# Kernel optimization log

Measured on AMD Instinct MI355X. Metric: run time of the kernel, lower is better.

Reference implementation:

```python
import jax, jax.numpy as jnp
import numpy as np

NUM_BLOCKS = 16  # 4x4 grid of 2x2 blocks over the 8x8 matrix
E_BLK, H_BLK = 4, 2
E_CROSS, H_CROSS = 64, 8
VOCAB = 32000
LN_EPS = 1e-5


def _mha(x, Wqkv, bqkv, Wo, bo, nheads):
    """torch nn.MultiheadAttention (batch_first, self-attn, eval mode).
    Returns (out [B,T,E], attn weights averaged over heads [B,T,T])."""
    B, T, E = x.shape
    Dh = E // nheads
    qkv = x @ Wqkv.T + bqkv                      # [B,T,3E]
    q, k, v = jnp.split(qkv, 3, axis=-1)
    sp = lambda t: t.reshape(B, T, nheads, Dh).transpose(0, 2, 1, 3)  # [B,H,T,Dh]
    q, k, v = sp(q), sp(k), sp(v)
    scale = 1.0 / float(np.sqrt(Dh))
    scores = jnp.einsum('bhqd,bhkd->bhqk', q, k) * scale
    attn = jax.nn.softmax(scores, axis=-1)
    out = jnp.einsum('bhqk,bhkd->bhqd', attn, v).transpose(0, 2, 1, 3).reshape(B, T, E)
    return out @ Wo.T + bo, attn.mean(axis=1)


def _layernorm(x, g, b):
    mu = x.mean(-1, keepdims=True)
    var = x.var(-1, keepdims=True)
    return (x - mu) * jax.lax.rsqrt(var + LN_EPS) * g + b


def _to_blocks(M):
    # [B,T,8,8] -> [B,T,16,4]; block i = (row_blk*4+col_blk), 2x2 flattened row-major
    B, T = M.shape[:2]
    return jnp.transpose(M.reshape(B, T, 4, 2, 4, 2), (0, 1, 2, 4, 3, 5)).reshape(B, T, 16, 4)


def _from_blocks(x):
    # [B,T,16,4] -> [B,T,8,8]
    B, T = x.shape[:2]
    return jnp.transpose(x.reshape(B, T, 4, 4, 2, 2), (0, 1, 2, 4, 3, 5)).reshape(B, T, 8, 8)


def setup_inputs() -> dict:
    key = jax.random.key(0)
    ks = jax.random.split(key, 24)
    B, T = 4, 1024
    s = 0.05
    return {
        'M': jax.random.normal(ks[0], (B, T, 8, 8), jnp.float32),
        'token_ids': jax.random.randint(ks[1], (B, T), 0, VOCAB, jnp.int64),
        # 16 per-block MHA param sets (stacked)
        'Wqkv_blk': jax.random.normal(ks[2], (NUM_BLOCKS, 3 * E_BLK, E_BLK), jnp.float32) * s,
        'bqkv_blk': jnp.zeros((NUM_BLOCKS, 3 * E_BLK), jnp.float32),
        'Wo_blk': jax.random.normal(ks[3], (NUM_BLOCKS, E_BLK, E_BLK), jnp.float32) * s,
        'bo_blk': jnp.zeros((NUM_BLOCKS, E_BLK), jnp.float32),
        # cross-block MHA
        'Wqkv_c': jax.random.normal(ks[4], (3 * E_CROSS, E_CROSS), jnp.float32) * s,
        'bqkv_c': jnp.zeros((3 * E_CROSS,), jnp.float32),
        'Wo_c': jax.random.normal(ks[5], (E_CROSS, E_CROSS), jnp.float32) * s,
        'bo_c': jnp.zeros((E_CROSS,), jnp.float32),
        # FFN 64 -> 256 -> 64
        'W1': jax.random.normal(ks[6], (256, 64), jnp.float32) * s,
        'b1': jnp.zeros((256,), jnp.float32),
        'W2': jax.random.normal(ks[7], (64, 256), jnp.float32) * s,
        'b2': jnp.zeros((64,), jnp.float32),
        # LayerNorms
        'g1': jnp.ones((64,), jnp.float32), 'be1': jnp.zeros((64,), jnp.float32),
        'g2': jnp.ones((64,), jnp.float32), 'be2': jnp.zeros((64,), jnp.float32),
        # DynamicBlockSensitivity params
        'sens_emb': jax.random.normal(ks[8], (VOCAB, NUM_BLOCKS), jnp.float32) * s,
        'sens_alpha': jax.random.normal(ks[9], (NUM_BLOCKS,), jnp.float32) * s,
    }


def reference(M, token_ids, Wqkv_blk, bqkv_blk, Wo_blk, bo_blk,
              Wqkv_c, bqkv_c, Wo_c, bo_c, W1, b1, W2, b2,
              g1, be1, g2, be2, sens_emb, sens_alpha):
    B, T = M.shape[:2]
    blocks = _to_blocks(M)                                # [B,T,16,4]
    x_blk = jnp.moveaxis(blocks, 2, 0)                    # [16,B,T,4]
    blk_out, _ = jax.vmap(lambda x, W, b, Wo, bo: _mha(x, W, b, Wo, bo, H_BLK))(
        x_blk, Wqkv_blk, bqkv_blk, Wo_blk, bo_blk)        # [16,B,T,4]
    all_blocks = jnp.moveaxis(blk_out, 0, 2).reshape(B, T, 64)
    cross_out, attn_w = _mha(all_blocks, Wqkv_c, bqkv_c, Wo_c, bo_c, H_CROSS)
    all_blocks = _layernorm(all_blocks + cross_out, g1, be1)
    ffn = jax.nn.gelu(all_blocks @ W1.T + b1, approximate=False) @ W2.T + b2
    all_blocks = _layernorm(all_blocks + ffn, g2, be2)
    # Dynamic block sensitivity: token embedding + attention-received modulation
    attn_recv = attn_w.mean(axis=1)                       # [B,T] attention each token receives
    sens = jax.nn.sigmoid(sens_emb[token_ids] + attn_recv[..., None] * sens_alpha)  # [B,T,16]
    new_blocks = blocks + (all_blocks.reshape(B, T, 16, 4) - blocks) * sens[..., None]
    return _from_blocks(new_blocks)
```

## Files before the change

### kernel.cpp

```cpp
#include <hip/hip_runtime.h>
#include <hip/hip_bf16.h>
#include <math.h>

#define BB 4
#define TT 1024
#define BT 4096

#define OFF_BLOCKS 0
#define OFF_QKVB   262144
#define OFF_RECVP  262144
#define OFF_ALLB   1048576
#define OFF_QKVC   1310720
#define OFF_LC     2097152
#define OFF_ACCC   2129920
#define OFF_LN1    2396160
#define OFF_PARAMS 2658304
#define WS_FLOATS  2708624

#define P_W1T    0
#define P_W2T    16384
#define P_WQCT   32768
#define P_WOCT   45056
#define P_WOBLK  49152
#define P_BOBLK  49408
#define P_BQC    49472
#define P_BOC    49664
#define P_G1     49728
#define P_BE1    49792
#define P_B1     49856
#define P_B2     50112
#define P_G2     50176
#define P_BE2    50240
#define P_SAL    50304
#define P_TOTAL  50320

__device__ inline float rcpf(float x) { return __builtin_amdgcn_rcpf(x); }

typedef _Float16 h2 __attribute__((ext_vector_type(2)));
typedef __fp16   fh2 __attribute__((ext_vector_type(2)));
typedef _Float16 h8v __attribute__((ext_vector_type(8)));
typedef float    f4v __attribute__((ext_vector_type(4)));

__device__ inline uint pkh(float a, float b) {
#if __has_builtin(__builtin_amdgcn_cvt_pkrtz)
  fh2 r = __builtin_amdgcn_cvt_pkrtz(a, b);
  return __builtin_bit_cast(uint, r);
#else
  h2 r = { (_Float16)a, (_Float16)b };
  return __builtin_bit_cast(uint, r);
#endif
}
__device__ inline h2 toh2(uint u) { return __builtin_bit_cast(h2, u); }

__device__ inline float dot2h(h2 a, h2 b, float c) {
#if __has_builtin(__builtin_amdgcn_fdot2)
  return __builtin_amdgcn_fdot2(a, b, c, false);
#else
  return c + (float)a.x * (float)b.x + (float)a.y * (float)b.y;
#endif
}

__device__ inline bool detect_bf16(const void* M) {
  const unsigned short* h = (const unsigned short*)M;
  unsigned short v = h[threadIdx.x & 63];
  int e = (v >> 7) & 0xff;
  unsigned long long m = __ballot((e >= 90) && (e <= 141));
  return __popcll(m) >= 58;
}

template <bool ISBF>
__device__ inline float ldf(const void* p, int i) {
  if (ISBF) return __bfloat162float(((const __hip_bfloat16*)p)[i]);
  else      return ((const float*)p)[i];
}

template <bool ISBF>
__device__ void prep2_body(
    const void* M, const void* Wqkv_blk, const void* bqkv_blk,
    const void* W1, const void* W2, const void* Wqkv_c, const void* Wo_c,
    const void* Wo_blk, const void* bo_blk, const void* bqkv_c, const void* bo_c,
    const void* g1, const void* be1, const void* b1, const void* b2,
    const void* g2, const void* be2, const void* sens_al,
    float* blocks, float* qkv_blk, float* params) {
  if (blockIdx.x < 256) {
    int g = blockIdx.x * 256 + threadIdx.x;
    int i = g >> 12, bt = g & 4095;
    int rb = i >> 2, cb = i & 3;
    float x[4];
    #pragma unroll
    for (int r = 0; r < 2; ++r)
      #pragma unroll
      for (int c = 0; c < 2; ++c)
        x[r*2+c] = ldf<ISBF>(M, bt*64 + (rb*2+r)*8 + cb*2 + c);
    float* bo = blocks + bt*64 + i*4;
    #pragma unroll
    for (int j = 0; j < 4; ++j) bo[j] = x[j];
    float* o = qkv_blk + (i*BT + bt) * 12;
    #pragma unroll
    for (int c = 0; c < 12; ++c) {
      float a = ldf<ISBF>(bqkv_blk, i*12 + c);
      #pragma unroll
      for (int j = 0; j < 4; ++j) a += ldf<ISBF>(Wqkv_blk, i*48 + c*4 + j) * x[j];
      o[c] = a;
    }
  } else {
    for (int o = (blockIdx.x - 256)*256 + threadIdx.x; o < P_TOTAL; o += 16*256) {
      float v;
      if      (o < 16384) { int j = o >> 8, h2_ = o & 255; v = ldf<ISBF>(W1, h2_*64 + j); }
      else if (o < 32768) { int q = o - 16384; int k = q >> 6, j = q & 63; v = ldf<ISBF>(W2, j*256 + k); }
      else if (o < 45056) { int q = o - 32768; int j = q / 192, c = q % 192; v = ldf<ISBF>(Wqkv_c, c*64 + j); }
      else if (o < 49152) { int q = o - 45056; int m = q >> 6, j = q & 63; v = ldf<ISBF>(Wo_c, j*64 + m); }
      else if (o < 49408) v = ldf<ISBF>(Wo_blk, o - 49152);
      else if (o < 49472) v = ldf<ISBF>(bo_blk, o - 49408);
      else if (o < 49664) v = ldf<ISBF>(bqkv_c, o - 49472);
      else if (o < 49728) v = ldf<ISBF>(bo_c,   o - 49664);
      else if (o < 49792) v = ldf<ISBF>(g1,     o - 49728);
      else if (o < 49856) v = ldf<ISBF>(be1,    o - 49792);
      else if (o < 50112) v = ldf<ISBF>(b1,     o - 49856);
      else if (o < 50176) v = ldf<ISBF>(b2,     o - 50112);
      else if (o < 50240) v = ldf<ISBF>(g2,     o - 50176);
      else if (o < 50304) v = ldf<ISBF>(be2,    o - 50240);
      else                v = ldf<ISBF>(sens_al, o - 50304);
      params[o] = v;
    }
  }
}

__global__ void __launch_bounds__(256) k_prep3(
    const void* __restrict__ M, const void* __restrict__ Wqkv_blk,
    const void* __restrict__ bqkv_blk,
    const void* __restrict__ W1, const void* __restrict__ W2,
    const void* __restrict__ Wqkv_c, const void* __restrict__ Wo_c,
    const void* __restrict__ Wo_blk, const void* __restrict__ bo_blk,
    const void* __restrict__ bqkv_c, const void* __restrict__ bo_c,
    const void* __restrict__ g1, const void* __restrict__ be1,
    const void* __restrict__ b1, const void* __restrict__ b2,
    const void* __restrict__ g2, const void* __restrict__ be2,
    const void* __restrict__ sens_al,
    float* __restrict__ blocks, float* __restrict__ qkv_blk,
    float* __restrict__ params) {
  if (detect_bf16(M))
    prep2_body<true >(M, Wqkv_blk, bqkv_blk, W1, W2, Wqkv_c, Wo_c, Wo_blk, bo_blk,
                      bqkv_c, bo_c, g1, be1, b1, b2, g2, be2, sens_al,
                      blocks, qkv_blk, params);
  else
    prep2_body<false>(M, Wqkv_blk, bqkv_blk, W1, W2, Wqkv_c, Wo_c, Wo_blk, bo_blk,
                      bqkv_c, bo_c, g1, be1, b1, b2, g2, be2, sens_al,
                      blocks, qkv_blk, params);
}

__global__ void __launch_bounds__(256) k_blk4(
    const float* __restrict__ qkv_blk,
    const float* __restrict__ params,
    float* __restrict__ all_blocks) {
  __shared__ __align__(16) uint lds[9236];
  uint* kvu = lds;
  uint* vt  = lds + 4096;
  ushort* vt16 = (ushort*)vt;
  int bid = blockIdx.x;
  int qc = bid & 15, b = (bid >> 4) & 3, i = bid >> 6;
  int tid = threadIdx.x;
  int wv = tid >> 6, lane = tid & 63;
  int lq = lane & 15, g = lane >> 4;
  const float* slab = qkv_blk + (size_t)(i*BT + b*TT) * 12;
  #pragma unroll
  for (int rr = 0; rr < 4; ++rr) {
    int r = tid + rr*256;
    const float4* rp = (const float4*)(slab + (size_t)r*12);
    float4 x1 = rp[1], x2 = rp[2];
    uint v01 = pkh(x2.x, x2.y), v23 = pkh(x2.z, x2.w);
    *(uint4*)(kvu + r*4) = make_uint4(pkh(x1.x,x1.y), pkh(x1.z,x1.w), v01, v23);
    vt16[0*1032 + r] = (ushort)(v01 & 0xffffu);
    vt16[1*1032 + r] = (ushort)(v01 >> 16);
    vt16[2*1032 + r] = (ushort)(v23 & 0xffffu);
    vt16[3*1032 + r] = (ushort)(v23 >> 16);
    vt16[4*1032 + r] = (ushort)0x3C00;
  }
  int qrow = qc*64 + wv*16 + lq;
  float4 qv = *(const float4*)(slab + (size_t)qrow*12);
  const float S2L = 0.70710678f * 1.44269504f;
  uint pq01 = pkh(qv.x*S2L, qv.y*S2L);
  uint pq23 = pkh(qv.z*S2L, qv.w*S2L);
  uint4 bq0u = make_uint4(g == 0 ? pq01 : 0u, 0u, 0u, 0u);
  uint4 bq1u = make_uint4(0u, g == 0 ? pq23 : 0u, 0u, 0u);
  h8v B0 = __builtin_bit_cast(h8v, bq0u);
  h8v B1 = __builtin_bit_cast(h8v, bq1u);
  __syncthreads();
  uint* pt0 = lds + 6676 + (wv*2 + 0)*320;
  uint* pt1 = lds + 6676 + (wv*2 + 1)*320;
  f4v acc0 = {0.f, 0.f, 0.f, 0.f};
  f4v acc1 = {0.f, 0.f, 0.f, 0.f};
  for (int c = 0; c < 32; ++c) {
    int kb = c*32;
    #pragma unroll
    for (int t = 0; t < 2; ++t) {
      uint4 aku = *(const uint4*)(kvu + (size_t)(kb + t*16 + lq)*4);
      h8v AK = __builtin_bit_cast(h8v, aku);
      f4v z = {0.f, 0.f, 0.f, 0.f};
      f4v s0 = __builtin_amdgcn_mfma_f32_16x16x32_f16(AK, B0, z, 0, 0, 0);
      f4v s1 = __builtin_amdgcn_mfma_f32_16x16x32_f16(AK, B1, z, 0, 0, 0);
      uint a01 = pkh(exp2f(s0[0]), exp2f(s0[1]));
      uint a23 = pkh(exp2f(s0[2]), exp2f(s0[3]));
      uint c01 = pkh(exp2f(s1[0]), exp2f(s1[1]));
      uint c23 = pkh(exp2f(s1[2]), exp2f(s1[3]));
      *(uint2*)(pt0 + lq*20 + t*8 + g*2) = make_uint2(a01, a23);
      *(uint2*)(pt1 + lq*20 + t*8 + g*2) = make_uint2(c01, c23);
    }
    uint4 avu = make_uint4(0u, 0u, 0u, 0u);
    if (lq < 5) avu = *(const uint4*)(vt + (size_t)lq*516 + c*16 + g*4);
    h8v AV = __builtin_bit_cast(h8v, avu);
    h8v BP0 = __builtin_bit_cast(h8v, *(const uint4*)(pt0 + lq*20 + g*4));
    h8v BP1 = __builtin_bit_cast(h8v, *(const uint4*)(pt1 + lq*20 + g*4));
    acc0 = __builtin_amdgcn_mfma_f32_16x16x32_f16(AV, BP0, acc0, 0, 0, 0);
    acc1 = __builtin_amdgcn_mfma_f32_16x16x32_f16(AV, BP1, acc1, 0, 0, 0);
  }
  float l0 = __shfl(acc0[0], 16 + lq);
  float l1 = __shfl(acc1[0], 16 + lq);
  if (g == 0) {
    float inv0 = rcpf(l0), inv1 = rcpf(l1);
    float o[4] = { acc0[0]*inv0, acc0[1]*inv0, acc1[2]*inv1, acc1[3]*inv1 };
    const float* pWo = params + P_WOBLK + i*16;
    float4 outv;
    #pragma unroll
    for (int j = 0; j < 4; ++j) {
      float a = params[P_BOBLK + i*4 + j];
      #pragma unroll
      for (int m2 = 0; m2 < 4; ++m2) a += pWo[j*4 + m2] * o[m2];
      ((float*)&outv)[j] = a;
    }
    *(float4*)(all_blocks + (size_t)(b*TT + qrow)*64 + i*4) = outv;
  }
}

__global__ void __launch_bounds__(256) k_qkv_c2(
    const float* __restrict__ all_blocks,
    const float* __restrict__ params,
    float* __restrict__ qkv_c) {
  __shared__ float w[12288];
  __shared__ float xs[256];
  int tid = threadIdx.x;
  int t0 = blockIdx.x * 4;
  {
    const float4* src = (const float4*)(params + P_WQCT);
    float4* dst = (float4*)w;
    #pragma unroll
    for (int i = tid; i < 3072; i += 256) dst[i] = src[i];
  }
  xs[tid] = all_blocks[t0*64 + tid];
  __syncthreads();
  int tt = tid >> 6, lane = tid & 63;
  int t = t0 + tt;
  const float* x = xs + tt*64;
  float a0 = params[P_BQC + lane];
  float a1 = params[P_BQC + 64 + lane];
  float a2 = params[P_BQC + 128 + lane];
  #pragma unroll 8
  for (int j = 0; j < 64; ++j) {
    const float* r = w + j*192;
    float xj = x[j];
    a0 += r[lane]       * xj;
    a1 += r[64 + lane]  * xj;
    a2 += r[128 + lane] * xj;
  }
  float* o = qkv_c + (size_t)t*192;
  o[lane] = a0; o[64 + lane] = a1; o[128 + lane] = a2;
}

__global__ void __launch_bounds__(1024) k_cross10(
    const float* __restrict__ qkv_c,
    float* __restrict__ acc_c,
    float* __restrict__ recv_part) {
  __shared__ __align__(16) uint lds[23680];
  uint*  Ku   = lds;
  uint*  Vu   = lds + 4096;
  float* red  = (float*)(lds + 4096);
  float* rcmb = (float*)(lds + 4096);
  uint*  qb_  = lds + 22656;
  int bid = blockIdx.x;
  int qt = bid & 7, h = (bid >> 3) & 7, b = bid >> 6;
  int tid = threadIdx.x;
  int wv = __builtin_amdgcn_readfirstlane(tid) >> 6;
  int ql = tid & 63;
  int h8 = h*8;
  const float* base = qkv_c + (size_t)b*TT*192;
  {
    int r = tid;
    const float4* kp = (const float4*)(base + (size_t)r*192 + 64 + h8);
    const float4* vp = (const float4*)(base + (size_t)r*192 + 128 + h8);
    float4 k0 = kp[0], k1 = kp[1], v0 = vp[0], v1 = vp[1];
    *(uint4*)(Ku + r*4) = make_uint4(pkh(k0.x,k0.y), pkh(k0.z,k0.w),
                                     pkh(k1.x,k1.y), pkh(k1.z,k1.w));
    *(uint4*)(Vu + r*4) = make_uint4(pkh(v0.x,v0.y), pkh(v0.z,v0.w),
                                     pkh(v1.x,v1.y), pkh(v1.z,v1.w));
  }
  int qa = qt*128 + ql, qbq = qa + 64;
  const float SCL = 0.35355339f * 1.44269504f;
  uint qa01,qa23,qa45,qa67, qb01,qb23,qb45,qb67;
  {
    const float4* pa = (const float4*)(base + (size_t)qa*192 + h8);
    const float4* pb = (const float4*)(base + (size_t)qbq*192 + h8);
    float4 a0 = pa[0], a1 = pa[1], b0 = pb[0], b1 = pb[1];
    qa01 = pkh(a0.x*SCL, a0.y*SCL); qa23 = pkh(a0.z*SCL, a0.w*SCL);
    qa45 = pkh(a1.x*SCL, a1.y*SCL); qa67 = pkh(a1.z*SCL, a1.w*SCL);
    qb01 = pkh(b0.x*SCL, b0.y*SCL); qb23 = pkh(b0.z*SCL, b0.w*SCL);
    qb45 = pkh(b1.x*SCL, b1.y*SCL); qb67 = pkh(b1.z*SCL, b1.w*SCL);
  }
  __syncthreads();
  float la = 0.f, lb = 0.f, aca[8], acb[8];
  #pragma unroll
  for (int c = 0; c < 8; ++c) { aca[c] = 0.f; acb[c] = 0.f; }
  int kbeg = wv*64;
  #pragma unroll 4
  for (int k = kbeg; k < kbeg + 64; ++k) {
    uint4 kk = *(const uint4*)(Ku + k*4);
    uint4 vv = *(const uint4*)(Vu + k*4);
    h2 k01 = toh2(kk.x), k23 = toh2(kk.y), k45 = toh2(kk.z), k67 = toh2(kk.w);
    float sa = dot2h(toh2(qa01),k01, dot2h(toh2(qa23),k23, 0.f))
             + dot2h(toh2(qa45),k45, dot2h(toh2(qa67),k67, 0.f));
    float sb = dot2h(toh2(qb01),k01, dot2h(toh2(qb23),k23, 0.f))
             + dot2h(toh2(qb45),k45, dot2h(toh2(qb67),k67, 0.f));
    float pa = exp2f(sa);
    float pb = exp2f(sb);
    la += pa; lb += pb;
    h2 v01 = toh2(vv.x), v23 = toh2(vv.y), v45 = toh2(vv.z), v67 = toh2(vv.w);
    aca[0] += pa*(float)v01.x; aca[1] += pa*(float)v01.y;
    aca[2] += pa*(float)v23.x; aca[3] += pa*(float)v23.y;
    aca[4] += pa*(float)v45.x; aca[5] += pa*(float)v45.y;
    aca[6] += pa*(float)v67.x; aca[7] += pa*(float)v67.y;
    acb[0] += pb*(float)v01.x; acb[1] += pb*(float)v01.y;
    acb[2] += pb*(float)v23.x; acb[3] += pb*(float)v23.y;
    acb[4] += pb*(float)v45.x; acb[5] += pb*(float)v45.y;
    acb[6] += pb*(float)v67.x; acb[7] += pb*(float)v67.y;
  }
  __syncthreads();
  {
    float* ra = red + ql*145 + wv*9;
    ra[0] = la;
    #pragma unroll
    for (int c = 0; c < 8; ++c) ra[1+c] = aca[c];
    float* rb = red + (ql+64)*145 + wv*9;
    rb[0] = lb;
    #pragma unroll
    for (int c = 0; c < 8; ++c) rb[1+c] = acb[c];
    if (wv == 0) {
      *(uint4*)(qb_ + ql*8)      = make_uint4(qa01, qa23, qa45, qa67);
      *(uint4*)(qb_ + (ql+64)*8) = make_uint4(qb01, qb23, qb45, qb67);
    }
  }
  __syncthreads();
  if (tid < 128) {
    float ls = 0.f, as[8];
    #pragma unroll
    for (int c = 0; c < 8; ++c) as[c] = 0.f;
    #pragma unroll
    for (int w = 0; w < 16; ++w) {
      const float* p = red + tid*145 + w*9;
      ls += p[0];
      #pragma unroll
      for (int c = 0; c < 8; ++c) as[c] += p[1+c];
    }
    float invl = rcpf(ls);
    int q2 = qt*128 + tid;
    int idx = (b*8 + h)*TT + q2;
    float4 o0 = { as[0]*invl, as[1]*invl, as[2]*invl, as[3]*invl };
    float4 o1 = { as[4]*invl, as[5]*invl, as[6]*invl, as[7]*invl };
    float4* op = (float4*)(acc_c + (size_t)idx*8);
    op[0] = o0; op[1] = o1;
    ((float*)(qb_ + tid*8))[4] = -__log2f(ls);
  }
  __syncthreads();
  {
    int qq = wv >> 2, g = wv & 3;
    int p = g*64 + ql;
    uint4 ka = *(const uint4*)(Ku + p*4);
    uint4 kb = *(const uint4*)(Ku + (p+256)*4);
    uint4 kc = *(const uint4*)(Ku + (p+512)*4);
    uint4 kd = *(const uint4*)(Ku + (p+768)*4);
    float r0 = 0.f, r1 = 0.f, r2 = 0.f, r3 = 0.f;
    const uint* qrow = qb_ + qq*32*8;
    #pragma unroll 4
    for (int q = 0; q < 32; ++q) {
      uint4 q4 = *(const uint4*)(qrow + q*8);
      float mq = __uint_as_float(qrow[q*8 + 4]);
      h2 Q0 = toh2(q4.x), Q1 = toh2(q4.y), Q2 = toh2(q4.z), Q3 = toh2(q4.w);
      float s0 = dot2h(Q0,toh2(ka.x), dot2h(Q1,toh2(ka.y), 0.f))
               + dot2h(Q2,toh2(ka.z), dot2h(Q3,toh2(ka.w), 0.f));
      float s1 = dot2h(Q0,toh2(kb.x), dot2h(Q1,toh2(kb.y), 0.f))
               + dot2h(Q2,toh2(kb.z), dot2h(Q3,toh2(kb.w), 0.f));
      float s2 = dot2h(Q0,toh2(kc.x), dot2h(Q1,toh2(kc.y), 0.f))
               + dot2h(Q2,toh2(kc.z), dot2h(Q3,toh2(kc.w), 0.f));
      float s3 = dot2h(Q0,toh2(kd.x), dot2h(Q1,toh2(kd.y), 0.f))
               + dot2h(Q2,toh2(kd.z), dot2h(Q3,toh2(kd.w), 0.f));
      r0 += exp2f(s0 + mq);
      r1 += exp2f(s1 + mq);
      r2 += exp2f(s2 + mq);
      r3 += exp2f(s3 + mq);
    }
    rcmb[(p      )*4 + qq] = r0;
    rcmb[(p + 256)*4 + qq] = r1;
    rcmb[(p + 512)*4 + qq] = r2;
    rcmb[(p + 768)*4 + qq] = r3;
  }
  __syncthreads();
  {
    int k = tid;
    float4 v = *(const float4*)(rcmb + k*4);
    int src = h*8 + qt;
    recv_part[((size_t)(b*1024 + k))*64 + src] = v.x + v.y + v.z + v.w;
  }
}

__global__ void __launch_bounds__(256) k_fin(
    const float* __restrict__ all_blocks,
    const float* __restrict__ acc_c,
    const float* __restrict__ params,
    float* __restrict__ ln1) {
  __shared__ float pvs[4*64];
  int tt = threadIdx.x >> 6, j = threadIdx.x & 63;
  int t = blockIdx.x*4 + tt;
  int b = t >> 10, tl = t & 1023;
  int h = j >> 3;
  int idx = (b*8 + h)*TT + tl;
  pvs[tt*64 + j] = acc_c[idx*8 + (j & 7)];
  __syncthreads();
  float a = params[P_BOC + j];
  const float* WoT = params + P_WOCT;
  const float* p = pvs + tt*64;
  #pragma unroll 8
  for (int m = 0; m < 64; ++m) a += WoT[m*64 + j] * p[m];
  float x = all_blocks[t*64 + j] + a;
  float s = x, s2 = x*x;
  #pragma unroll
  for (int off = 32; off; off >>= 1) { s += __shfl_xor(s, off); s2 += __shfl_xor(s2, off); }
  float mu  = s  * (1.f/64.f);
  float var = s2 * (1.f/64.f) - mu*mu;
  float y = (x - mu) * rsqrtf(var + 1e-5f) * params[P_G1 + j] + params[P_BE1 + j];
  ln1[t*64 + j] = y;
}

template <bool ISBF>
__device__ void ffn_body(
    const float* ln1, const float* params, const float* blocks,
    const int* tok32, const float* recv_part, const void* sens_emb, void* out,
    float* w, float* ld2, float* hbuf) {
  int tid = threadIdx.x;
  int t0 = blockIdx.x * 8;
  int wv = tid >> 6, lane = tid & 63;
  float recv;
  {
    int t = t0 + wv, b = t >> 10, k = t & 1023;
    const float* rp = recv_part + ((size_t)(b*1024 + k))*64;
    float s = rp[lane];
    #pragma unroll
    for (int off = 32; off; off >>= 1) s += __shfl_xor(s, off);
    recv = s * (1.f/8192.f);
  }
  ld2[lane*8 + wv] = ln1[(t0 + wv)*64 + lane];
  {
    const float4* src = (const float4*)(params + P_W1T);
    float4* dst = (float4*)w;
    #pragma unroll
    for (int i = tid; i < 4096; i += 512) dst[i] = src[i];
  }
  __syncthreads();
  {
    int g = tid >> 8, u = tid & 255;
    float a0, a1, a2, a3;
    a0 = a1 = a2 = a3 = params[P_B1 + u];
    #pragma unroll 8
    for (int j = 0; j < 64; ++j) {
      float wj = w[j*256 + u];
      float4 xj = *(const float4*)(ld2 + j*8 + g*4);
      a0 += wj*xj.x; a1 += wj*xj.y; a2 += wj*xj.z; a3 += wj*xj.w;
    }
    float av[4] = {a0, a1, a2, a3};
    float4 hv;
    #pragma unroll
    for (int t2 = 0; t2 < 4; ++t2) {
      float v = av[t2];
      float u2 = 1.5957691f*v + 0.07135481f*v*v*v;
      ((float*)&hv)[t2] = v * rcpf(1.f + __expf(-u2));
    }
    *(float4*)(hbuf + u*8 + g*4) = hv;
  }
  __syncthreads();
  {
    const float4* src = (const float4*)(params + P_W2T);
    float4* dst = (float4*)w;
    #pragma unroll
    for (int i = tid; i < 4096; i += 512) dst[i] = src[i];
  }
  __syncthreads();
  float yp[8] = {0.f,0.f,0.f,0.f,0.f,0.f,0.f,0.f};
  {
    int j = lane, k0 = wv*32;
    #pragma unroll 8
    for (int k = k0; k < k0 + 32; ++k) {
      float wkj = w[k*64 + j];
      float4 h03 = *(const float4*)(hbuf + k*8);
      float4 h47 = *(const float4*)(hbuf + k*8 + 4);
      yp[0] += wkj*h03.x; yp[1] += wkj*h03.y; yp[2] += wkj*h03.z; yp[3] += wkj*h03.w;
      yp[4] += wkj*h47.x; yp[5] += wkj*h47.y; yp[6] += wkj*h47.z; yp[7] += wkj*h47.w;
    }
  }
  __syncthreads();
  float* red2 = w;
  {
    #pragma unroll
    for (int t2 = 0; t2 < 8; ++t2) red2[wv*520 + t2*64 + lane] = yp[t2];
  }
  __syncthreads();
  int j = lane;
  int tok = wv;
  int t = t0 + tok, b = t >> 10;
  float y = params[P_B2 + j];
  #pragma unroll
  for (int wq = 0; wq < 8; ++wq) y += red2[wq*520 + tok*64 + j];
  float z = ld2[j*8 + tok] + y;
  float s = z, s2 = z*z;
  #pragma unroll
  for (int off = 32; off; off >>= 1) { s += __shfl_xor(s, off); s2 += __shfl_xor(s2, off); }
  float mu  = s  * (1.f/64.f);
  float var = s2 * (1.f/64.f) - mu*mu;
  float y2 = (z - mu) * rsqrtf(var + 1e-5f) * params[P_G2 + j] + params[P_BE2 + j];
  bool is64 = ((tok32[1] | tok32[3] | tok32[5] | tok32[7]) == 0);
  int tk = is64 ? tok32[t*2] : tok32[t];
  int i = j >> 2, e = j & 3;
  float sv = ldf<ISBF>(sens_emb, tk*16 + i) + recv * params[P_SAL + i];
  float sg = rcpf(1.f + __expf(-sv));
  float blk = blocks[t*64 + j];
  float nb = blk + (y2 - blk) * sg;
  int rb = i >> 2, cb = i & 3, r = e >> 1, c = e & 1;
  int oidx = t*64 + (rb*2 + r)*8 + cb*2 + c;
  if (ISBF) ((__hip_bfloat16*)out)[oidx] = __float2bfloat16(nb);
  else      ((float*)out)[oidx] = nb;
}

__global__ void __launch_bounds__(512) k_ffn_out3(
    const void* __restrict__ M,
    const float* __restrict__ ln1,
    const float* __restrict__ params,
    const float* __restrict__ blocks,
    const int* __restrict__ tok32,
    const float* __restrict__ recv_part,
    const void* __restrict__ sens_emb,
    void* __restrict__ out) {
  __shared__ float w[16384];
  __shared__ float ld2[512];
  __shared__ float hbuf[2048];
  if (detect_bf16(M))
    ffn_body<true >(ln1, params, blocks, tok32, recv_part, sens_emb, out, w, ld2, hbuf);
  else
    ffn_body<false>(ln1, params, blocks, tok32, recv_part, sens_emb, out, w, ld2, hbuf);
}

extern "C" void kernel_launch(void* const* d_in, const int* in_sizes, int n_in,
                              void* d_out, int out_size, void* d_ws, size_t ws_size,
                              hipStream_t stream) {
  const void* M        = d_in[0];
  const int*  tok      = (const int*)d_in[1];
  const void* Wqkv_blk = d_in[2];
  const void* bqkv_blk = d_in[3];
  const void* Wo_blk   = d_in[4];
  const void* bo_blk   = d_in[5];
  const void* Wqkv_c   = d_in[6];
  const void* bqkv_c   = d_in[7];
  const void* Wo_c     = d_in[8];
  const void* bo_c     = d_in[9];
  const void* W1       = d_in[10];
  const void* b1       = d_in[11];
  const void* W2       = d_in[12];
  const void* b2       = d_in[13];
  const void* g1       = d_in[14];
  const void* be1      = d_in[15];
  const void* g2i      = d_in[16];
  const void* be2      = d_in[17];
  const void* sens_emb = d_in[18];
  const void* sens_al  = d_in[19];

  float* ws = (float*)d_ws;
  float* blocks    = ws + OFF_BLOCKS;
  float* qkv_blk   = ws + OFF_QKVB;
  float* recv_part = ws + OFF_RECVP;
  float* all_blk   = ws + OFF_ALLB;
  float* qkv_c     = ws + OFF_QKVC;
  float* acc_c     = ws + OFF_ACCC;
  float* ln1       = ws + OFF_LN1;
  float* params    = ws + OFF_PARAMS;

  k_prep3<<<272, 256, 0, stream>>>(M, Wqkv_blk, bqkv_blk, W1, W2, Wqkv_c, Wo_c,
                                   Wo_blk, bo_blk, bqkv_c, bo_c, g1, be1, b1, b2,
                                   g2i, be2, sens_al, blocks, qkv_blk, params);
  k_blk4<<<1024, 256, 0, stream>>>(qkv_blk, params, all_blk);
  k_qkv_c2<<<1024, 256, 0, stream>>>(all_blk, params, qkv_c);
  k_cross10<<<256, 1024, 0, stream>>>(qkv_c, acc_c, recv_part);
  k_fin<<<1024, 256, 0, stream>>>(all_blk, acc_c, params, ln1);
  k_ffn_out3<<<512, 512, 0, stream>>>(M, ln1, params, blocks, tok, recv_part,
                                      sens_emb, (void*)d_out);
}
```

Before: 208.0 us.

## Rewrite cross-block attention with MFMA f16 matrix instructions for QK and PV

Replaces the scalar fdot2-based cross attention kernel with one using 16x16x32 f16 MFMA for QK^T scores, PV accumulation (with a ones row in transposed V to get the softmax denominator), and the attention-received recomputation pass. The grid changes to 512 blocks of 256 threads, each handling 64 queries per (batch, head), and the per-source receive partials widen from 64 to 128 columns, with the consumer kernel updated to match. The aim is to move the dominant dot-product work onto matrix cores. The trade-off is wasted MFMA lanes from zero padding, since head dim 8 only fills a quarter of K, plus LDS round-trips for P and shuffle reductions.

```diff
diff --git a/kernel.cpp b/kernel.cpp
--- a/kernel.cpp
+++ b/kernel.cpp
@@ -51,14 +51,6 @@
 #endif
 }
 __device__ inline h2 toh2(uint u) { return __builtin_bit_cast(h2, u); }
-
-__device__ inline float dot2h(h2 a, h2 b, float c) {
-#if __has_builtin(__builtin_amdgcn_fdot2)
-  return __builtin_amdgcn_fdot2(a, b, c, false);
-#else
-  return c + (float)a.x * (float)b.x + (float)a.y * (float)b.y;
-#endif
-}
 
 __device__ inline bool detect_bf16(const void* M) {
   const unsigned short* h = (const unsigned short*)M;
@@ -266,147 +258,125 @@
   o[lane] = a0; o[64 + lane] = a1; o[128 + lane] = a2;
 }
 
-__global__ void __launch_bounds__(1024) k_cross10(
+__global__ void __launch_bounds__(256) k_cross11(
     const float* __restrict__ qkv_c,
     float* __restrict__ acc_c,
     float* __restrict__ recv_part) {
-  __shared__ __align__(16) uint lds[23680];
-  uint*  Ku   = lds;
-  uint*  Vu   = lds + 4096;
-  float* red  = (float*)(lds + 4096);
-  float* rcmb = (float*)(lds + 4096);
-  uint*  qb_  = lds + 22656;
+  __shared__ __align__(16) uint lds[14116];
+  uint* Ku = lds;
+  uint* Vt = lds + 4096;
+  ushort* vt16 = (ushort*)Vt;
+  float* rcv = (float*)(lds + 10020);
   int bid = blockIdx.x;
-  int qt = bid & 7, h = (bid >> 3) & 7, b = bid >> 6;
+  int h = bid & 7, b = (bid >> 3) & 3, qc = bid >> 5;
   int tid = threadIdx.x;
-  int wv = __builtin_amdgcn_readfirstlane(tid) >> 6;
-  int ql = tid & 63;
+  int wv = tid >> 6, lane = tid & 63;
+  int lq = lane & 15, g = lane >> 4;
   int h8 = h*8;
   const float* base = qkv_c + (size_t)b*TT*192;
-  {
-    int r = tid;
+  #pragma unroll
+  for (int rr = 0; rr < 4; ++rr) {
+    int r = tid + rr*256;
     const float4* kp = (const float4*)(base + (size_t)r*192 + 64 + h8);
     const float4* vp = (const float4*)(base + (size_t)r*192 + 128 + h8);
     float4 k0 = kp[0], k1 = kp[1], v0 = vp[0], v1 = vp[1];
     *(uint4*)(Ku + r*4) = make_uint4(pkh(k0.x,k0.y), pkh(k0.z,k0.w),
                                      pkh(k1.x,k1.y), pkh(k1.z,k1.w));
-    *(uint4*)(Vu + r*4) = make_uint4(pkh(v0.x,v0.y), pkh(v0.z,v0.w),
-                                     pkh(v1.x,v1.y), pkh(v1.z,v1.w));
-  }
-  int qa = qt*128 + ql, qbq = qa + 64;
+    uint v01 = pkh(v0.x,v0.y), v23 = pkh(v0.z,v0.w);
+    uint v45 = pkh(v1.x,v1.y), v67 = pkh(v1.z,v1.w);
+    vt16[0*1032 + r] = (ushort)(v01 & 0xffffu);
+    vt16[1*1032 + r] = (ushort)(v01 >> 16);
+    vt16[2*1032 + r] = (ushort)(v23 & 0xffffu);
+    vt16[3*1032 + r] = (ushort)(v23 >> 16);
+    vt16[4*1032 + r] = (ushort)(v45 & 0xffffu);
+    vt16[5*1032 + r] = (ushort)(v45 >> 16);
+    vt16[6*1032 + r] = (ushort)(v67 & 0xffffu);
+    vt16[7*1032 + r] = (ushort)(v67 >> 16);
+    vt16[8*1032 + r] = (ushort)0x3C00;
+  }
+  int q2 = qc*64 + wv*16 + lq;
   const float SCL = 0.35355339f * 1.44269504f;
-  uint qa01,qa23,qa45,qa67, qb01,qb23,qb45,qb67;
-  {
-    const float4* pa = (const float4*)(base + (size_t)qa*192 + h8);
-    const float4* pb = (const float4*)(base + (size_t)qbq*192 + h8);
-    float4 a0 = pa[0], a1 = pa[1], b0 = pb[0], b1 = pb[1];
-    qa01 = pkh(a0.x*SCL, a0.y*SCL); qa23 = pkh(a0.z*SCL, a0.w*SCL);
-    qa45 = pkh(a1.x*SCL, a1.y*SCL); qa67 = pkh(a1.z*SCL, a1.w*SCL);
-    qb01 = pkh(b0.x*SCL, b0.y*SCL); qb23 = pkh(b0.z*SCL, b0.w*SCL);
-    qb45 = pkh(b1.x*SCL, b1.y*SCL); qb67 = pkh(b1.z*SCL, b1.w*SCL);
-  }
-  __syncthreads();
-  float la = 0.f, lb = 0.f, aca[8], acb[8];
-  #pragma unroll
-  for (int c = 0; c < 8; ++c) { aca[c] = 0.f; acb[c] = 0.f; }
-  int kbeg = wv*64;
-  #pragma unroll 4
-  for (int k = kbeg; k < kbeg + 64; ++k) {
-    uint4 kk = *(const uint4*)(Ku + k*4);
-    uint4 vv = *(const uint4*)(Vu + k*4);
-    h2 k01 = toh2(kk.x), k23 = toh2(kk.y), k45 = toh2(kk.z), k67 = toh2(kk.w);
-    float sa = dot2h(toh2(qa01),k01, dot2h(toh2(qa23),k23, 0.f))
-             + dot2h(toh2(qa45),k45, dot2h(toh2(qa67),k67, 0.f));
-    float sb = dot2h(toh2(qb01),k01, dot2h(toh2(qb23),k23, 0.f))
-             + dot2h(toh2(qb45),k45, dot2h(toh2(qb67),k67, 0.f));
-    float pa = exp2f(sa);
-    float pb = exp2f(sb);
-    la += pa; lb += pb;
-    h2 v01 = toh2(vv.x), v23 = toh2(vv.y), v45 = toh2(vv.z), v67 = toh2(vv.w);
-    aca[0] += pa*(float)v01.x; aca[1] += pa*(float)v01.y;
-    aca[2] += pa*(float)v23.x; aca[3] += pa*(float)v23.y;
-    aca[4] += pa*(float)v45.x; aca[5] += pa*(float)v45.y;
-    aca[6] += pa*(float)v67.x; aca[7] += pa*(float)v67.y;
-    acb[0] += pb*(float)v01.x; acb[1] += pb*(float)v01.y;
-    acb[2] += pb*(float)v23.x; acb[3] += pb*(float)v23.y;
-    acb[4] += pb*(float)v45.x; acb[5] += pb*(float)v45.y;
-    acb[6] += pb*(float)v67.x; acb[7] += pb*(float)v67.y;
-  }
-  __syncthreads();
-  {
-    float* ra = red + ql*145 + wv*9;
-    ra[0] = la;
-    #pragma unroll
-    for (int c = 0; c < 8; ++c) ra[1+c] = aca[c];
-    float* rb = red + (ql+64)*145 + wv*9;
-    rb[0] = lb;
-    #pragma unroll
-    for (int c = 0; c < 8; ++c) rb[1+c] = acb[c];
-    if (wv == 0) {
-      *(uint4*)(qb_ + ql*8)      = make_uint4(qa01, qa23, qa45, qa67);
-      *(uint4*)(qb_ + (ql+64)*8) = make_uint4(qb01, qb23, qb45, qb67);
-    }
-  }
-  __syncthreads();
-  if (tid < 128) {
-    float ls = 0.f, as[8];
-    #pragma unroll
-    for (int c = 0; c < 8; ++c) as[c] = 0.f;
-    #pragma unroll
-    for (int w = 0; w < 16; ++w) {
-      const float* p = red + tid*145 + w*9;
-      ls += p[0];
-      #pragma unroll
-      for (int c = 0; c < 8; ++c) as[c] += p[1+c];
-    }
-    float invl = rcpf(ls);
-    int q2 = qt*128 + tid;
+  uint4 bqu = make_uint4(0u, 0u, 0u, 0u);
+  {
+    const float4* qp = (const float4*)(base + (size_t)q2*192 + h8);
+    float4 q0 = qp[0], q1 = qp[1];
+    if (g == 0)
+      bqu = make_uint4(pkh(q0.x*SCL, q0.y*SCL), pkh(q0.z*SCL, q0.w*SCL),
+                       pkh(q1.x*SCL, q1.y*SCL), pkh(q1.z*SCL, q1.w*SCL));
+  }
+  h8v BQ = __builtin_bit_cast(h8v, bqu);
+  __syncthreads();
+  uint* pt = lds + 8740 + wv*320;
+  const uint4 zu4 = make_uint4(0u, 0u, 0u, 0u);
+  f4v acc = {0.f, 0.f, 0.f, 0.f};
+  for (int c = 0; c < 32; ++c) {
+    #pragma unroll
+    for (int t = 0; t < 2; ++t) {
+      uint4 aku = (g == 0) ? *(const uint4*)(Ku + (size_t)(c*32 + t*16 + lq)*4) : zu4;
+      h8v AK = __builtin_bit_cast(h8v, aku);
+      f4v z = {0.f, 0.f, 0.f, 0.f};
+      f4v s = __builtin_amdgcn_mfma_f32_16x16x32_f16(AK, BQ, z, 0, 0, 0);
+      uint e01 = pkh(exp2f(s[0]), exp2f(s[1]));
+      uint e23 = pkh(exp2f(s[2]), exp2f(s[3]));
+      *(uint2*)(pt + lq*20 + t*8 + g*2) = make_uint2(e01, e23);
+    }
+    uint4 avu = (lq < 9) ? *(const uint4*)(Vt + (size_t)lq*516 + c*16 + g*4) : zu4;
+    h8v AV = __builtin_bit_cast(h8v, avu);
+    h8v BP = __builtin_bit_cast(h8v, *(const uint4*)(pt + lq*20 + g*4));
+    acc = __builtin_amdgcn_mfma_f32_16x16x32_f16(AV, BP, acc, 0, 0, 0);
+  }
+  float l = __shfl(acc[0], 32 + lq);
+  float invl = rcpf(l);
+  float mq = -__log2f(l);
+  {
     int idx = (b*8 + h)*TT + q2;
-    float4 o0 = { as[0]*invl, as[1]*invl, as[2]*invl, as[3]*invl };
-    float4 o1 = { as[4]*invl, as[5]*invl, as[6]*invl, as[7]*invl };
-    float4* op = (float4*)(acc_c + (size_t)idx*8);
-    op[0] = o0; op[1] = o1;
-    ((float*)(qb_ + tid*8))[4] = -__log2f(ls);
-  }
-  __syncthreads();
-  {
-    int qq = wv >> 2, g = wv & 3;
-    int p = g*64 + ql;
-    uint4 ka = *(const uint4*)(Ku + p*4);
-    uint4 kb = *(const uint4*)(Ku + (p+256)*4);
-    uint4 kc = *(const uint4*)(Ku + (p+512)*4);
-    uint4 kd = *(const uint4*)(Ku + (p+768)*4);
-    float r0 = 0.f, r1 = 0.f, r2 = 0.f, r3 = 0.f;
-    const uint* qrow = qb_ + qq*32*8;
-    #pragma unroll 4
-    for (int q = 0; q < 32; ++q) {
-      uint4 q4 = *(const uint4*)(qrow + q*8);
-      float mq = __uint_as_float(qrow[q*8 + 4]);
-      h2 Q0 = toh2(q4.x), Q1 = toh2(q4.y), Q2 = toh2(q4.z), Q3 = toh2(q4.w);
-      float s0 = dot2h(Q0,toh2(ka.x), dot2h(Q1,toh2(ka.y), 0.f))
-               + dot2h(Q2,toh2(ka.z), dot2h(Q3,toh2(ka.w), 0.f));
-      float s1 = dot2h(Q0,toh2(kb.x), dot2h(Q1,toh2(kb.y), 0.f))
-               + dot2h(Q2,toh2(kb.z), dot2h(Q3,toh2(kb.w), 0.f));
-      float s2 = dot2h(Q0,toh2(kc.x), dot2h(Q1,toh2(kc.y), 0.f))
-               + dot2h(Q2,toh2(kc.z), dot2h(Q3,toh2(kc.w), 0.f));
-      float s3 = dot2h(Q0,toh2(kd.x), dot2h(Q1,toh2(kd.y), 0.f))
-               + dot2h(Q2,toh2(kd.z), dot2h(Q3,toh2(kd.w), 0.f));
-      r0 += exp2f(s0 + mq);
-      r1 += exp2f(s1 + mq);
-      r2 += exp2f(s2 + mq);
-      r3 += exp2f(s3 + mq);
-    }
-    rcmb[(p      )*4 + qq] = r0;
-    rcmb[(p + 256)*4 + qq] = r1;
-    rcmb[(p + 512)*4 + qq] = r2;
-    rcmb[(p + 768)*4 + qq] = r3;
-  }
-  __syncthreads();
-  {
-    int k = tid;
-    float4 v = *(const float4*)(rcmb + k*4);
-    int src = h*8 + qt;
-    recv_part[((size_t)(b*1024 + k))*64 + src] = v.x + v.y + v.z + v.w;
+    if (g == 0) {
+      float4 o = { acc[0]*invl, acc[1]*invl, acc[2]*invl, acc[3]*invl };
+      *(float4*)(acc_c + (size_t)idx*8) = o;
+    } else if (g == 1) {
+      float4 o = { acc[0]*invl, acc[1]*invl, acc[2]*invl, acc[3]*invl };
+      *(float4*)(acc_c + (size_t)idx*8 + 4) = o;
+    }
+  }
+  float* rcvw = rcv + wv*1024;
+  for (int x = lane; x < 1024; x += 64) rcvw[x] = 0.f;
+  for (int c2 = 0; c2 < 64; ++c2) {
+    uint4 aku = (g == 0) ? *(const uint4*)(Ku + (size_t)(c2*16 + lq)*4) : zu4;
+    h8v AK = __builtin_bit_cast(h8v, aku);
+    f4v z = {0.f, 0.f, 0.f, 0.f};
+    f4v s = __builtin_amdgcn_mfma_f32_16x16x32_f16(AK, BQ, z, 0, 0, 0);
+    float p0 = exp2f(s[0] + mq);
+    float p1 = exp2f(s[1] + mq);
+    float p2 = exp2f(s[2] + mq);
+    float p3 = exp2f(s[3] + mq);
+    #pragma unroll
+    for (int off = 1; off < 16; off <<= 1) {
+      p0 += __shfl_xor(p0, off);
+      p1 += __shfl_xor(p1, off);
+      p2 += __shfl_xor(p2, off);
+      p3 += __shfl_xor(p3, off);
+    }
+    if (lq == 0) {
+      int kb2 = c2*16 + g*4;
+      rcvw[kb2 + 0] += p0;
+      rcvw[kb2 + 1] += p1;
+      rcvw[kb2 + 2] += p2;
+      rcvw[kb2 + 3] += p3;
+    }
+  }
+  __syncthreads();
+  {
+    int k = tid*4;
+    float4 a0 = *(const float4*)(rcv + 0*1024 + k);
+    float4 a1 = *(const float4*)(rcv + 1*1024 + k);
+    float4 a2 = *(const float4*)(rcv + 2*1024 + k);
+    float4 a3 = *(const float4*)(rcv + 3*1024 + k);
+    int src = h*16 + qc;
+    size_t bk = ((size_t)(b*1024 + k))*128 + src;
+    recv_part[bk      ] = a0.x + a1.x + a2.x + a3.x;
+    recv_part[bk + 128] = a0.y + a1.y + a2.y + a3.y;
+    recv_part[bk + 256] = a0.z + a1.z + a2.z + a3.z;
+    recv_part[bk + 384] = a0.w + a1.w + a2.w + a3.w;
   }
 }
 
@@ -449,8 +419,8 @@
   float recv;
   {
     int t = t0 + wv, b = t >> 10, k = t & 1023;
-    const float* rp = recv_part + ((size_t)(b*1024 + k))*64;
-    float s = rp[lane];
+    const float* rp = recv_part + ((size_t)(b*1024 + k))*128;
+    float s = rp[lane] + rp[lane + 64];
     #pragma unroll
     for (int off = 32; off; off >>= 1) s += __shfl_xor(s, off);
     recv = s * (1.f/8192.f);
@@ -593,7 +563,7 @@
                                    g2i, be2, sens_al, blocks, qkv_blk, params);
   k_blk4<<<1024, 256, 0, stream>>>(qkv_blk, params, all_blk);
   k_qkv_c2<<<1024, 256, 0, stream>>>(all_blk, params, qkv_c);
-  k_cross10<<<256, 1024, 0, stream>>>(qkv_c, acc_c, recv_part);
+  k_cross11<<<512, 256, 0, stream>>>(qkv_c, acc_c, recv_part);
   k_fin<<<1024, 256, 0, stream>>>(all_blk, acc_c, params, ln1);
   k_ffn_out3<<<512, 512, 0, stream>>>(M, ln1, params, blocks, tok, recv_part,
                                       sens_emb, (void*)d_out);
```

Measured after the change: 221.8 us. +6.6%, slower.

## Compute cross-attention QKV projection with fp16 MFMA over 16-token tiles

Applied to the files above, without the earlier changes.

Replaces the scalar fp32 QKV projection with a kernel that packs the weights to fp16 in LDS and uses 16x16x32 MFMA instructions, handling 16 tokens per block instead of 4. This cuts the per-block reload of the full weight matrix and the scalar FMA cost. In exchange, inputs and weights are rounded to fp16, which reduces accuracy, and each block still transposes and packs the weights itself.

```diff
diff --git a/kernel.cpp b/kernel.cpp
--- a/kernel.cpp
+++ b/kernel.cpp
@@ -232,38 +232,48 @@
   }
 }
 
-__global__ void __launch_bounds__(256) k_qkv_c2(
+__global__ void __launch_bounds__(256) k_qkv_c3(
     const float* __restrict__ all_blocks,
     const float* __restrict__ params,
     float* __restrict__ qkv_c) {
-  __shared__ float w[12288];
-  __shared__ float xs[256];
+  __shared__ __align__(16) uint wt[6912];
   int tid = threadIdx.x;
-  int t0 = blockIdx.x * 4;
-  {
-    const float4* src = (const float4*)(params + P_WQCT);
-    float4* dst = (float4*)w;
-    #pragma unroll
-    for (int i = tid; i < 3072; i += 256) dst[i] = src[i];
-  }
-  xs[tid] = all_blocks[t0*64 + tid];
-  __syncthreads();
-  int tt = tid >> 6, lane = tid & 63;
-  int t = t0 + tt;
-  const float* x = xs + tt*64;
-  float a0 = params[P_BQC + lane];
-  float a1 = params[P_BQC + 64 + lane];
-  float a2 = params[P_BQC + 128 + lane];
-  #pragma unroll 8
-  for (int j = 0; j < 64; ++j) {
-    const float* r = w + j*192;
-    float xj = x[j];
-    a0 += r[lane]       * xj;
-    a1 += r[64 + lane]  * xj;
-    a2 += r[128 + lane] * xj;
-  }
-  float* o = qkv_c + (size_t)t*192;
-  o[lane] = a0; o[64 + lane] = a1; o[128 + lane] = a2;
+  int wv = tid >> 6, lane = tid & 63;
+  int lq = lane & 15, g = lane >> 4;
+  for (int o = tid; o < 6144; o += 256) {
+    int c = o % 192, jp = o / 192;
+    float w0 = params[P_WQCT + (2*jp    )*192 + c];
+    float w1 = params[P_WQCT + (2*jp + 1)*192 + c];
+    wt[c*36 + jp] = pkh(w0, w1);
+  }
+  int t0 = blockIdx.x * 16;
+  const float* xr = all_blocks + (size_t)(t0 + lq)*64;
+  uint4 a0u, a1u;
+  {
+    float4 x0 = *(const float4*)(xr + 8*g);
+    float4 x1 = *(const float4*)(xr + 8*g + 4);
+    a0u = make_uint4(pkh(x0.x,x0.y), pkh(x0.z,x0.w), pkh(x1.x,x1.y), pkh(x1.z,x1.w));
+    float4 x2 = *(const float4*)(xr + 32 + 8*g);
+    float4 x3 = *(const float4*)(xr + 32 + 8*g + 4);
+    a1u = make_uint4(pkh(x2.x,x2.y), pkh(x2.z,x2.w), pkh(x3.x,x3.y), pkh(x3.z,x3.w));
+  }
+  h8v A0 = __builtin_bit_cast(h8v, a0u);
+  h8v A1 = __builtin_bit_cast(h8v, a1u);
+  __syncthreads();
+  #pragma unroll
+  for (int nt = 0; nt < 3; ++nt) {
+    int ct = wv*3 + nt;
+    int c = ct*16 + lq;
+    h8v Bw0 = __builtin_bit_cast(h8v, *(const uint4*)(wt + c*36 + g*4));
+    h8v Bw1 = __builtin_bit_cast(h8v, *(const uint4*)(wt + c*36 + 16 + g*4));
+    f4v acc = {0.f, 0.f, 0.f, 0.f};
+    acc = __builtin_amdgcn_mfma_f32_16x16x32_f16(A0, Bw0, acc, 0, 0, 0);
+    acc = __builtin_amdgcn_mfma_f32_16x16x32_f16(A1, Bw1, acc, 0, 0, 0);
+    float bias = params[P_BQC + c];
+    #pragma unroll
+    for (int r = 0; r < 4; ++r)
+      qkv_c[(size_t)(t0 + 4*g + r)*192 + c] = acc[r] + bias;
+  }
 }
 
 __global__ void __launch_bounds__(1024) k_cross10(
@@ -592,7 +602,7 @@
                                    Wo_blk, bo_blk, bqkv_c, bo_c, g1, be1, b1, b2,
                                    g2i, be2, sens_al, blocks, qkv_blk, params);
   k_blk4<<<1024, 256, 0, stream>>>(qkv_blk, params, all_blk);
-  k_qkv_c2<<<1024, 256, 0, stream>>>(all_blk, params, qkv_c);
+  k_qkv_c3<<<256, 256, 0, stream>>>(all_blk, params, qkv_c);
   k_cross10<<<256, 1024, 0, stream>>>(qkv_c, acc_c, recv_part);
   k_fin<<<1024, 256, 0, stream>>>(all_blk, acc_c, params, ln1);
   k_ffn_out3<<<512, 512, 0, stream>>>(M, ln1, params, blocks, tok, recv_part,
```

Measured after the change: 209.9 us. Within noise of the previous version (+0.9%).
